# Performance work log

Measured on AMD Instinct MI355X. Metric: run time of the kernel, lower is better.

The kernel has to match this reference:

```python
import jax, jax.numpy as jnp
import numpy as np

B, S, D = 131072, 30, 4
Q = 16  # q_size for both branches
V1, V2 = 21, 11


def setup_inputs() -> dict:
    key = jax.random.key(0)
    ks = jax.random.split(key, 13)
    s = 0.5  # small init scale (~1/sqrt(in))
    inp = {
        "x": jax.random.normal(ks[0], (B, S, D), dtype=jnp.float32),
        # branch 1 (v_size=21)
        "q1_w": jax.random.normal(ks[1], (D, Q), dtype=jnp.float32) * s,
        "q1_b": jax.random.normal(ks[2], (Q,), dtype=jnp.float32) * s,
        "k1_w": jax.random.normal(ks[3], (D, Q), dtype=jnp.float32) * s,
        "k1_b": jax.random.normal(ks[4], (Q,), dtype=jnp.float32) * s,
        "v1_w": jax.random.normal(ks[5], (D, V1), dtype=jnp.float32) * s,
        "v1_b": jax.random.normal(ks[6], (V1,), dtype=jnp.float32) * s,
        # branch 2 (v_size=11)
        "q2_w": jax.random.normal(ks[7], (D, Q), dtype=jnp.float32) * s,
        "q2_b": jax.random.normal(ks[8], (Q,), dtype=jnp.float32) * s,
        "k2_w": jax.random.normal(ks[9], (D, Q), dtype=jnp.float32) * s,
        "k2_b": jax.random.normal(ks[10], (Q,), dtype=jnp.float32) * s,
        "v2_w": jax.random.normal(ks[11], (D, V2), dtype=jnp.float32) * s,
        "v2_b": jax.random.normal(ks[12], (V2,), dtype=jnp.float32) * s,
    }
    return inp


def _attn(x, qw, qb, kw, kb, vw, vb):
    # x: [B, S, D]; unscaled softmax attention + tanh (faithful to source)
    q = jnp.einsum("bsd,dq->bsq", x, qw) + qb  # [B,S,Q]
    k = jnp.einsum("bsd,dq->bsq", x, kw) + kb  # [B,S,Q]
    v = jnp.einsum("bsd,dv->bsv", x, vw) + vb  # [B,S,V]
    scores = jnp.einsum("bsq,btq->bst", q, k)  # [B,S,S], no 1/sqrt(d) scaling
    attn = jax.nn.softmax(scores, axis=-1)
    out = jnp.einsum("bst,btv->bsv", attn, v)
    return jnp.tanh(out)


def reference(x, q1_w, q1_b, k1_w, k1_b, v1_w, v1_b,
              q2_w, q2_b, k2_w, k2_b, v2_w, v2_b):
    num = _attn(x, q1_w, q1_b, k1_w, k1_b, v1_w, v1_b)  # [B,S,21]
    t = _attn(x, q2_w, q2_b, k2_w, k2_b, v2_w, v2_b)    # [B,S,11]
    return (num, t)
```

## Files before the change

kernel.cpp:

```cpp
#include <hip/hip_runtime.h>

#define SS 30
#define QQ 16
#define NV1 21
#define NV2 11
#define NVT 32
#define NBPB 4
#define ROWS (NBPB * SS)
#define THREADS 64

#define LOG2E 1.44269504088896340736f

typedef float v2f __attribute__((ext_vector_type(2)));
typedef float v4f __attribute__((ext_vector_type(4)));

__device__ __forceinline__ v2f bcast(float x) { v2f r; r.x = x; r.y = x; return r; }
__device__ __forceinline__ v2f pkfma(v2f a, v2f b, v2f c) {
    return __builtin_elementwise_fma(a, b, c);
}

__global__ __launch_bounds__(64) void precompute_consts(
    const float* __restrict__ q1w, const float* __restrict__ q1b,
    const float* __restrict__ k1w,
    const float* __restrict__ q2w, const float* __restrict__ q2b,
    const float* __restrict__ k2w,
    const float* __restrict__ v1w, const float* __restrict__ v1b,
    const float* __restrict__ v2w, const float* __restrict__ v2b,
    float* __restrict__ ws)
{
    const int tid = threadIdx.x;
    if (tid < 40) {
        const int br = tid / 20, idx = tid % 20;
        const float* qw = br ? q2w : q1w;
        const float* qb = br ? q2b : q1b;
        const float* kw = br ? k2w : k1w;
        float acc = 0.f;
        if (idx < 16) {
            const int d = idx >> 2, e = idx & 3;
            #pragma unroll
            for (int q = 0; q < QQ; ++q) acc += qw[d * QQ + q] * kw[e * QQ + q];
        } else {
            const int e = idx - 16;
            #pragma unroll
            for (int q = 0; q < QQ; ++q) acc += kw[e * QQ + q] * qb[q];
        }
        ws[tid] = acc * LOG2E;
    }
    if (tid < NVT) {
        const float s2l = 2.0f * LOG2E;
        v4f w; float b;
        if (tid < NV1) {
            w.x = v1w[tid] * s2l;          w.y = v1w[NV1 + tid] * s2l;
            w.z = v1w[2 * NV1 + tid] * s2l; w.w = v1w[3 * NV1 + tid] * s2l;
            b = v1b[tid] * s2l;
        } else {
            const int p = tid - NV1;
            w.x = v2w[p] * s2l;            w.y = v2w[NV2 + p] * s2l;
            w.z = v2w[2 * NV2 + p] * s2l;  w.w = v2w[3 * NV2 + p] * s2l;
            b = v2b[p] * s2l;
        }
        reinterpret_cast<v4f*>(ws + 40)[tid] = w;
        ws[168 + tid] = b;
    }
}

__global__ __launch_bounds__(THREADS, 4) void fused_dual_attn(
    const float* __restrict__ x, const float* __restrict__ ws,
    float* __restrict__ out1, float* __restrict__ out2)
{
    __shared__ float cm[40];
    __shared__ v4f  vwt[NVT];
    __shared__ float vbl[NVT];
    __shared__ v4f  xsv[ROWS];
    __shared__ alignas(16) float stage[ROWS * NV1];

    const int tid = threadIdx.x;
    const long long blk = blockIdx.x;

    if (tid < 40) cm[tid] = ws[tid];
    if (tid < NVT) {
        vwt[tid] = reinterpret_cast<const v4f*>(ws + 40)[tid];
        vbl[tid] = ws[168 + tid];
    }
    {
        const v4f* xg = reinterpret_cast<const v4f*>(x) + blk * ROWS;
        xsv[tid] = __builtin_nontemporal_load(xg + tid);
        if (tid < ROWS - 64) xsv[64 + tid] = __builtin_nontemporal_load(xg + 64 + tid);
    }
    __syncthreads();

    int lrowA = 0, lrowB = 0;
    v2f h1p[4], h2p[4];
    if (tid < 60) {
        const int batch = (unsigned)tid / 15;
        const int sA = tid - batch * 15;
        lrowA = batch * SS + sA;
        lrowB = lrowA + 15;
        const v4f* xb = xsv + batch * SS;
        const v4f xA = xsv[lrowA];
        const v4f xB = xsv[lrowB];

        v2f g1p[4], g2p[4];
        #pragma unroll
        for (int e = 0; e < 4; ++e) {
            g1p[e].x = cm[16 + e] + xA.x * cm[e] + xA.y * cm[4 + e]
                     + xA.z * cm[8 + e] + xA.w * cm[12 + e];
            g1p[e].y = cm[16 + e] + xB.x * cm[e] + xB.y * cm[4 + e]
                     + xB.z * cm[8 + e] + xB.w * cm[12 + e];
            g2p[e].x = cm[36 + e] + xA.x * cm[20 + e] + xA.y * cm[24 + e]
                     + xA.z * cm[28 + e] + xA.w * cm[32 + e];
            g2p[e].y = cm[36 + e] + xB.x * cm[20 + e] + xB.y * cm[24 + e]
                     + xB.z * cm[28 + e] + xB.w * cm[32 + e];
        }

        v2f sum1 = {0.f, 0.f}, sum2 = {0.f, 0.f};
        #pragma unroll
        for (int e = 0; e < 4; ++e) { h1p[e] = sum1; h2p[e] = sum1; }

        #pragma unroll
        for (int t = 0; t < SS; ++t) {
            const v4f xt = xb[t];
            const v2f bx = bcast(xt.x), by = bcast(xt.y), bz = bcast(xt.z), bw = bcast(xt.w);
            v2f s1 = g1p[3] * bw;
            s1 = pkfma(g1p[2], bz, s1);
            s1 = pkfma(g1p[1], by, s1);
            s1 = pkfma(g1p[0], bx, s1);
            v2f s2 = g2p[3] * bw;
            s2 = pkfma(g2p[2], bz, s2);
            s2 = pkfma(g2p[1], by, s2);
            s2 = pkfma(g2p[0], bx, s2);
            v2f p1, p2;
            p1.x = __builtin_amdgcn_exp2f(s1.x);
            p1.y = __builtin_amdgcn_exp2f(s1.y);
            p2.x = __builtin_amdgcn_exp2f(s2.x);
            p2.y = __builtin_amdgcn_exp2f(s2.y);
            sum1 = sum1 + p1;
            sum2 = sum2 + p2;
            h1p[0] = pkfma(p1, bx, h1p[0]);
            h1p[1] = pkfma(p1, by, h1p[1]);
            h1p[2] = pkfma(p1, bz, h1p[2]);
            h1p[3] = pkfma(p1, bw, h1p[3]);
            h2p[0] = pkfma(p2, bx, h2p[0]);
            h2p[1] = pkfma(p2, by, h2p[1]);
            h2p[2] = pkfma(p2, bz, h2p[2]);
            h2p[3] = pkfma(p2, bw, h2p[3]);
        }
        v2f inv1, inv2;
        inv1.x = __builtin_amdgcn_rcpf(sum1.x);
        inv1.y = __builtin_amdgcn_rcpf(sum1.y);
        inv2.x = __builtin_amdgcn_rcpf(sum2.x);
        inv2.y = __builtin_amdgcn_rcpf(sum2.y);
        #pragma unroll
        for (int e = 0; e < 4; ++e) { h1p[e] = h1p[e] * inv1; h2p[e] = h2p[e] * inv2; }
    }

    if (tid < 60) {
        float* sA = stage + lrowA * NV1;
        float* sB = stage + lrowB * NV1;
        #pragma unroll
        for (int o = 0; o < NV1; ++o) {
            const v4f w = vwt[o];
            v2f sp = bcast(vbl[o]);
            sp = pkfma(h1p[3], bcast(w.w), sp);
            sp = pkfma(h1p[2], bcast(w.z), sp);
            sp = pkfma(h1p[1], bcast(w.y), sp);
            sp = pkfma(h1p[0], bcast(w.x), sp);
            v2f ex;
            ex.x = __builtin_amdgcn_exp2f(sp.x);
            ex.y = __builtin_amdgcn_exp2f(sp.y);
            sA[o] = fmaf(-2.0f, __builtin_amdgcn_rcpf(ex.x + 1.0f), 1.0f);
            sB[o] = fmaf(-2.0f, __builtin_amdgcn_rcpf(ex.y + 1.0f), 1.0f);
        }
    }
    __syncthreads();
    {
        const int n1 = ROWS * NV1 / 4;
        v4f* dst1 = reinterpret_cast<v4f*>(out1) + blk * n1;
        const v4f* src = reinterpret_cast<const v4f*>(stage);
        for (int i = tid; i < n1; i += THREADS)
            __builtin_nontemporal_store(src[i], dst1 + i);
    }
    __syncthreads();

    if (tid < 60) {
        float* sA = stage + lrowA * NV2;
        float* sB = stage + lrowB * NV2;
        #pragma unroll
        for (int o = 0; o < NV2; ++o) {
            const v4f w = vwt[NV1 + o];
            v2f sp = bcast(vbl[NV1 + o]);
            sp = pkfma(h2p[3], bcast(w.w), sp);
            sp = pkfma(h2p[2], bcast(w.z), sp);
            sp = pkfma(h2p[1], bcast(w.y), sp);
            sp = pkfma(h2p[0], bcast(w.x), sp);
            v2f ex;
            ex.x = __builtin_amdgcn_exp2f(sp.x);
            ex.y = __builtin_amdgcn_exp2f(sp.y);
            sA[o] = fmaf(-2.0f, __builtin_amdgcn_rcpf(ex.x + 1.0f), 1.0f);
            sB[o] = fmaf(-2.0f, __builtin_amdgcn_rcpf(ex.y + 1.0f), 1.0f);
        }
    }
    __syncthreads();
    {
        const int n2 = ROWS * NV2 / 4;
        v4f* dst2 = reinterpret_cast<v4f*>(out2) + blk * n2;
        const v4f* src = reinterpret_cast<const v4f*>(stage);
        for (int i = tid; i < n2; i += THREADS)
            __builtin_nontemporal_store(src[i], dst2 + i);
    }
}

extern "C" void kernel_launch(void* const* d_in, const int* in_sizes, int n_in,
                              void* d_out, int out_size, void* d_ws, size_t ws_size,
                              hipStream_t stream) {
    const float* x   = (const float*)d_in[0];
    const float* q1w = (const float*)d_in[1];
    const float* q1b = (const float*)d_in[2];
    const float* k1w = (const float*)d_in[3];
    const float* v1w = (const float*)d_in[5];
    const float* v1b = (const float*)d_in[6];
    const float* q2w = (const float*)d_in[7];
    const float* q2b = (const float*)d_in[8];
    const float* k2w = (const float*)d_in[9];
    const float* v2w = (const float*)d_in[11];
    const float* v2b = (const float*)d_in[12];

    const long long B = 131072LL;
    float* out1 = (float*)d_out;
    float* out2 = out1 + B * SS * NV1;
    float* ws   = (float*)d_ws;

    precompute_consts<<<1, 64, 0, stream>>>(q1w, q1b, k1w, q2w, q2b, k2w,
                                            v1w, v1b, v2w, v2b, ws);

    const int nblocks = (int)(B / NBPB);
    fused_dual_attn<<<nblocks, THREADS, 0, stream>>>(x, ws, out1, out2);
}
```

Baseline: 145.5 us.

## Pack both branches per thread and halve batches per block

```diff
diff --git a/kernel.cpp b/kernel.cpp
--- a/kernel.cpp
+++ b/kernel.cpp
@@ -5,7 +5,7 @@
 #define NV1 21
 #define NV2 11
 #define NVT 32
-#define NBPB 4
+#define NBPB 2
 #define ROWS (NBPB * SS)
 #define THREADS 64
 
@@ -64,7 +64,7 @@
     }
 }
 
-__global__ __launch_bounds__(THREADS, 4) void fused_dual_attn(
+__global__ __launch_bounds__(THREADS, 8) void fused_dual_attn(
     const float* __restrict__ x, const float* __restrict__ ws,
     float* __restrict__ out1, float* __restrict__ out2)
 {
@@ -82,94 +82,64 @@
         vwt[tid] = reinterpret_cast<const v4f*>(ws + 40)[tid];
         vbl[tid] = ws[168 + tid];
     }
-    {
+    if (tid < ROWS) {
         const v4f* xg = reinterpret_cast<const v4f*>(x) + blk * ROWS;
         xsv[tid] = __builtin_nontemporal_load(xg + tid);
-        if (tid < ROWS - 64) xsv[64 + tid] = __builtin_nontemporal_load(xg + 64 + tid);
-    }
-    __syncthreads();
-
-    int lrowA = 0, lrowB = 0;
-    v2f h1p[4], h2p[4];
-    if (tid < 60) {
-        const int batch = (unsigned)tid / 15;
-        const int sA = tid - batch * 15;
-        lrowA = batch * SS + sA;
-        lrowB = lrowA + 15;
+    }
+    __syncthreads();
+
+    v2f hp[4] = {{0.f,0.f},{0.f,0.f},{0.f,0.f},{0.f,0.f}};
+    if (tid < ROWS) {
+        const int batch = (tid >= SS) ? 1 : 0;
         const v4f* xb = xsv + batch * SS;
-        const v4f xA = xsv[lrowA];
-        const v4f xB = xsv[lrowB];
-
-        v2f g1p[4], g2p[4];
+        const v4f xr = xsv[tid];
+
+        v2f g[4];
         #pragma unroll
         for (int e = 0; e < 4; ++e) {
-            g1p[e].x = cm[16 + e] + xA.x * cm[e] + xA.y * cm[4 + e]
-                     + xA.z * cm[8 + e] + xA.w * cm[12 + e];
-            g1p[e].y = cm[16 + e] + xB.x * cm[e] + xB.y * cm[4 + e]
-                     + xB.z * cm[8 + e] + xB.w * cm[12 + e];
-            g2p[e].x = cm[36 + e] + xA.x * cm[20 + e] + xA.y * cm[24 + e]
-                     + xA.z * cm[28 + e] + xA.w * cm[32 + e];
-            g2p[e].y = cm[36 + e] + xB.x * cm[20 + e] + xB.y * cm[24 + e]
-                     + xB.z * cm[28 + e] + xB.w * cm[32 + e];
-        }
-
-        v2f sum1 = {0.f, 0.f}, sum2 = {0.f, 0.f};
-        #pragma unroll
-        for (int e = 0; e < 4; ++e) { h1p[e] = sum1; h2p[e] = sum1; }
-
+            g[e].x = cm[16 + e] + xr.x * cm[e] + xr.y * cm[4 + e]
+                   + xr.z * cm[8 + e] + xr.w * cm[12 + e];
+            g[e].y = cm[36 + e] + xr.x * cm[20 + e] + xr.y * cm[24 + e]
+                   + xr.z * cm[28 + e] + xr.w * cm[32 + e];
+        }
+
+        v2f sum = {0.f, 0.f};
         #pragma unroll
         for (int t = 0; t < SS; ++t) {
             const v4f xt = xb[t];
             const v2f bx = bcast(xt.x), by = bcast(xt.y), bz = bcast(xt.z), bw = bcast(xt.w);
-            v2f s1 = g1p[3] * bw;
-            s1 = pkfma(g1p[2], bz, s1);
-            s1 = pkfma(g1p[1], by, s1);
-            s1 = pkfma(g1p[0], bx, s1);
-            v2f s2 = g2p[3] * bw;
-            s2 = pkfma(g2p[2], bz, s2);
-            s2 = pkfma(g2p[1], by, s2);
-            s2 = pkfma(g2p[0], bx, s2);
-            v2f p1, p2;
-            p1.x = __builtin_amdgcn_exp2f(s1.x);
-            p1.y = __builtin_amdgcn_exp2f(s1.y);
-            p2.x = __builtin_amdgcn_exp2f(s2.x);
-            p2.y = __builtin_amdgcn_exp2f(s2.y);
-            sum1 = sum1 + p1;
-            sum2 = sum2 + p2;
-            h1p[0] = pkfma(p1, bx, h1p[0]);
-            h1p[1] = pkfma(p1, by, h1p[1]);
-            h1p[2] = pkfma(p1, bz, h1p[2]);
-            h1p[3] = pkfma(p1, bw, h1p[3]);
-            h2p[0] = pkfma(p2, bx, h2p[0]);
-            h2p[1] = pkfma(p2, by, h2p[1]);
-            h2p[2] = pkfma(p2, bz, h2p[2]);
-            h2p[3] = pkfma(p2, bw, h2p[3]);
-        }
-        v2f inv1, inv2;
-        inv1.x = __builtin_amdgcn_rcpf(sum1.x);
-        inv1.y = __builtin_amdgcn_rcpf(sum1.y);
-        inv2.x = __builtin_amdgcn_rcpf(sum2.x);
-        inv2.y = __builtin_amdgcn_rcpf(sum2.y);
-        #pragma unroll
-        for (int e = 0; e < 4; ++e) { h1p[e] = h1p[e] * inv1; h2p[e] = h2p[e] * inv2; }
-    }
-
-    if (tid < 60) {
-        float* sA = stage + lrowA * NV1;
-        float* sB = stage + lrowB * NV1;
+            v2f s = g[3] * bw;
+            s = pkfma(g[2], bz, s);
+            s = pkfma(g[1], by, s);
+            s = pkfma(g[0], bx, s);
+            v2f p;
+            p.x = __builtin_amdgcn_exp2f(s.x);
+            p.y = __builtin_amdgcn_exp2f(s.y);
+            sum = sum + p;
+            hp[0] = pkfma(p, bx, hp[0]);
+            hp[1] = pkfma(p, by, hp[1]);
+            hp[2] = pkfma(p, bz, hp[2]);
+            hp[3] = pkfma(p, bw, hp[3]);
+        }
+        v2f inv;
+        inv.x = __builtin_amdgcn_rcpf(sum.x);
+        inv.y = __builtin_amdgcn_rcpf(sum.y);
+        #pragma unroll
+        for (int e = 0; e < 4; ++e) hp[e] = hp[e] * inv;
+    }
+
+    if (tid < ROWS) {
+        float* sp = stage + tid * NV1;
         #pragma unroll
         for (int o = 0; o < NV1; ++o) {
             const v4f w = vwt[o];
-            v2f sp = bcast(vbl[o]);
-            sp = pkfma(h1p[3], bcast(w.w), sp);
-            sp = pkfma(h1p[2], bcast(w.z), sp);
-            sp = pkfma(h1p[1], bcast(w.y), sp);
-            sp = pkfma(h1p[0], bcast(w.x), sp);
-            v2f ex;
-            ex.x = __builtin_amdgcn_exp2f(sp.x);
-            ex.y = __builtin_amdgcn_exp2f(sp.y);
-            sA[o] = fmaf(-2.0f, __builtin_amdgcn_rcpf(ex.x + 1.0f), 1.0f);
-            sB[o] = fmaf(-2.0f, __builtin_amdgcn_rcpf(ex.y + 1.0f), 1.0f);
+            float v = vbl[o];
+            v = fmaf(hp[0].x, w.x, v);
+            v = fmaf(hp[1].x, w.y, v);
+            v = fmaf(hp[2].x, w.z, v);
+            v = fmaf(hp[3].x, w.w, v);
+            const float ex = __builtin_amdgcn_exp2f(v);
+            sp[o] = fmaf(-2.0f, __builtin_amdgcn_rcpf(ex + 1.0f), 1.0f);
         }
     }
     __syncthreads();
@@ -182,22 +152,18 @@
     }
     __syncthreads();
 
-    if (tid < 60) {
-        float* sA = stage + lrowA * NV2;
-        float* sB = stage + lrowB * NV2;
+    if (tid < ROWS) {
+        float* sp = stage + tid * NV2;
         #pragma unroll
         for (int o = 0; o < NV2; ++o) {
             const v4f w = vwt[NV1 + o];
-            v2f sp = bcast(vbl[NV1 + o]);
-            sp = pkfma(h2p[3], bcast(w.w), sp);
-            sp = pkfma(h2p[2], bcast(w.z), sp);
-            sp = pkfma(h2p[1], bcast(w.y), sp);
-            sp = pkfma(h2p[0], bcast(w.x), sp);
-            v2f ex;
-            ex.x = __builtin_amdgcn_exp2f(sp.x);
-            ex.y = __builtin_amdgcn_exp2f(sp.y);
-            sA[o] = fmaf(-2.0f, __builtin_amdgcn_rcpf(ex.x + 1.0f), 1.0f);
-            sB[o] = fmaf(-2.0f, __builtin_amdgcn_rcpf(ex.y + 1.0f), 1.0f);
+            float v = vbl[NV1 + o];
+            v = fmaf(hp[0].y, w.x, v);
+            v = fmaf(hp[1].y, w.y, v);
+            v = fmaf(hp[2].y, w.z, v);
+            v = fmaf(hp[3].y, w.w, v);
+            const float ex = __builtin_amdgcn_exp2f(v);
+            sp[o] = fmaf(-2.0f, __builtin_amdgcn_rcpf(ex + 1.0f), 1.0f);
         }
     }
     __syncthreads();
```

Result: no change. 145.0 us (-0.4%).
